# Optimization experiments

Hardware: AMD Instinct MI355X
Metric: run time of the kernel (lower is better)

Reference implementation:

```python
import jax, jax.numpy as jnp
import numpy as np

B, S, I, H, O = 64, 512, 256, 1024, 128

def setup_inputs() -> dict:
    key = jax.random.key(0)
    ks = jax.random.split(key, 9)
    s_in = 1.0 / np.sqrt(I)
    s_h = 1.0 / np.sqrt(H)
    return {
        "x": jax.random.normal(ks[0], (B, S, I), dtype=jnp.float32),
        "W_in": jax.random.uniform(ks[1], (H, I), jnp.float32, -s_in, s_in),
        "b_in": jax.random.uniform(ks[2], (H,), jnp.float32, -s_in, s_in),
        "W_rec": jax.random.uniform(ks[3], (H, H), jnp.float32, -s_h, s_h),
        "b_rec": jax.random.uniform(ks[4], (H,), jnp.float32, -s_h, s_h),
        "tau_m": jnp.full((H,), 2.0, dtype=jnp.float32),
        "tau_n": jnp.full((H,), 2.0, dtype=jnp.float32),
        "W_out": jax.random.uniform(ks[5], (O, H), jnp.float32, -s_h, s_h),
        "b_out": jax.random.uniform(ks[6], (O,), jnp.float32, -s_h, s_h),
    }

def reference(x, W_in, b_in, W_rec, b_rec, tau_m, tau_n, W_out, b_out):
    b, s, _ = x.shape
    h = W_in.shape[0]
    alpha = jax.nn.sigmoid(tau_m)  # [H]
    beta = jax.nn.sigmoid(tau_n)   # [H]
    # Precompute feedforward GEMM for all timesteps at once: [B,S,H]
    ff = jnp.einsum('bsi,hi->bsh', x, W_in) + b_in

    def step(carry, ff_t):
        mem, d, prev_spike = carry  # each [B,H]
        total = ff_t + prev_spike @ W_rec.T + b_rec
        d = beta * d + (1.0 - beta) * total
        mem = alpha * mem + (1.0 - alpha) * d
        spike = (mem > 1.0).astype(mem.dtype)
        mem = mem * (1.0 - spike)
        out = jax.nn.sigmoid(spike @ W_out.T + b_out)  # [B,O]
        return (mem, d, spike), out

    zeros = jnp.zeros((b, h), dtype=x.dtype)
    _, outs = jax.lax.scan(step, (zeros, zeros, zeros), jnp.swapaxes(ff, 0, 1))
    return jnp.swapaxes(outs, 0, 1)  # [B,S,O]
```

## Files before the change

kernel.cpp:

```cpp
#include <hip/hip_runtime.h>
#include <hip/hip_bf16.h>
#include <stdint.h>

#define B_ 64
#define S_ 512
#define I_ 256
#define H_ 1024
#define O_ 128
#define M_ (B_*S_)

typedef float f32x4 __attribute__((ext_vector_type(4)));

__global__ void __launch_bounds__(256) k0_convert(
    const float* __restrict__ x, const float* __restrict__ Win,
    uint8_t* __restrict__ xf8, uint8_t* __restrict__ wf8)
{
    __shared__ unsigned lds32[64 * 65];
    const int i = blockIdx.x;
    const int t = threadIdx.x;

    const float* src;
    uint8_t* dstBase;
    int kqStride;
    if (i < 512) {
        const int r0 = i * 64;
        src = x + (size_t)r0 * 256;
        const int T = i >> 1;
        const int rbase = (i & 1) * 4;
        dstBase = xf8 + (size_t)T * 32768 + rbase * 512;
        kqStride = 4096;
    } else {
        const int i2 = i - 512;
        src = Win + (size_t)(i2 * 64) * 256;
        dstBase = wf8 + (size_t)i2 * 16384;
        kqStride = 2048;
    }

#pragma unroll
    for (int j = 0; j < 16; ++j) {
        const int f = j * 256 + t;
        const int lrow = f >> 6, c4 = f & 63;
        float4 v = *(const float4*)(src + (size_t)lrow * 256 + c4 * 4);
        int w0 = 0;
        w0 = __builtin_amdgcn_cvt_pk_fp8_f32(v.x, v.y, w0, false);
        w0 = __builtin_amdgcn_cvt_pk_fp8_f32(v.z, v.w, w0, true);
        lds32[lrow * 65 + c4] = (unsigned)w0;
    }
    __syncthreads();

#pragma unroll
    for (int j = 0; j < 4; ++j) {
        const int c = j * 256 + t;
        const int kq  = c >> 7;
        const int rem = c & 127;
        const int rbl = rem >> 5;
        const int l0  = (rem & 31) * 2;
        const int r   = l0 & 15;
        const int q   = l0 >> 4;
        const int lrow = rbl * 16 + r;
        const int c0 = kq * 8 + q * 2;
        uint4 o;
        o.x = lds32[lrow * 65 + c0];
        o.y = lds32[lrow * 65 + c0 + 1];
        o.z = lds32[(lrow + 1) * 65 + c0];
        o.w = lds32[(lrow + 1) * 65 + c0 + 1];
        *(uint4*)(dstBase + kq * kqStride + rbl * 512 + l0 * 8) = o;
    }
}

__global__ void __launch_bounds__(256, 4) kf_gemm_scan(
    const uint8_t* __restrict__ xf8, const uint8_t* __restrict__ wf8,
    const float* __restrict__ b_in, const float* __restrict__ b_rec,
    const float* __restrict__ tau_m, const float* __restrict__ tau_n,
    const float* __restrict__ b_out,
    unsigned* __restrict__ crossed,
    float* __restrict__ out)
{
    __shared__ float lsf[128 * 68];

    const int tid  = threadIdx.x;
    const int w    = tid >> 6;
    const int lane = tid & 63;
    const int idx  = blockIdx.x;
    const int b    = (idx & 7) | ((idx >> 7) << 3);
    const int hn   = (idx >> 3) & 15;
    const int colrow = lane & 15;
    const int quad   = lane >> 4;

    float alpha = 0.f, beta = 0.f, cbr = 0.f, oma = 0.f, ombr = 0.f;
    float d = 0.f, mem = 0.f, mx = -1.0f;
    if (tid < 64) {
        const int hs = hn * 64 + tid;
        alpha = 1.f / (1.f + expf(-tau_m[hs]));
        beta  = 1.f / (1.f + expf(-tau_n[hs]));
        oma = 1.f - alpha; ombr = 1.f - beta;
        cbr = ombr * (b_in[hs] + b_rec[hs]);
    }

    const uint8_t* wB = wf8 + (size_t)hn * 16384 + lane * 8;
    long long bq[32];
#pragma unroll
    for (int kq = 0; kq < 8; ++kq)
#pragma unroll
        for (int ni = 0; ni < 4; ++ni)
            bq[kq * 4 + ni] = *(const long long*)(wB + kq * 2048 + ni * 512);

    for (int tt = 0; tt < 4; ++tt) {
        const uint8_t* xA = xf8 + (size_t)(b * 4 + tt) * 32768
                          + w * 1024 + lane * 8;

        f32x4 acc[2][4];
#pragma unroll
        for (int mi = 0; mi < 2; ++mi)
#pragma unroll
            for (int ni = 0; ni < 4; ++ni)
                acc[mi][ni] = (f32x4){0.f, 0.f, 0.f, 0.f};

#pragma unroll
        for (int kq = 0; kq < 8; ++kq) {
            long long a[2];
#pragma unroll
            for (int mi = 0; mi < 2; ++mi)
                a[mi] = *(const long long*)(xA + kq * 4096 + mi * 512);
#pragma unroll
            for (int mi = 0; mi < 2; ++mi)
#pragma unroll
                for (int ni = 0; ni < 4; ++ni)
                    acc[mi][ni] = __builtin_amdgcn_mfma_f32_16x16x32_fp8_fp8(
                        a[mi], bq[kq * 4 + ni], acc[mi][ni], 0, 0, 0);
        }

        __syncthreads();

#pragma unroll
        for (int mi = 0; mi < 2; ++mi) {
            const int t0 = w * 32 + mi * 16 + quad * 4;
#pragma unroll
            for (int ni = 0; ni < 4; ++ni) {
                const int h0 = ni * 16 + colrow;
                float* p = lsf + t0 * 68 + h0;
                p[0]   = acc[mi][ni][0];
                p[68]  = acc[mi][ni][1];
                p[136] = acc[mi][ni][2];
                p[204] = acc[mi][ni][3];
            }
        }
        __syncthreads();

        if (tid < 64) {
            for (int tl0 = 0; tl0 < 128; tl0 += 16) {
                float f[16];
#pragma unroll
                for (int u = 0; u < 16; ++u)
                    f[u] = lsf[(tl0 + u) * 68 + tid];
#pragma unroll
                for (int u = 0; u < 16; ++u) {
                    d   = fmaf(beta,  d,   fmaf(ombr, f[u], cbr));
                    mem = fmaf(alpha, mem, oma * d);
                    mx  = fmaxf(mx, mem);
                }
            }
        }
    }

    if (tid < 64) {
        unsigned long long bal = __ballot(mx > 1.0f);
        if (tid == 0) crossed[b * 16 + hn] = (bal != 0ull) ? 1u : 0u;
    }

    float4 v = *(const float4*)(b_out + (tid & 31) * 4);
    float4 r;
    r.x = 1.f / (1.f + expf(-v.x));
    r.y = 1.f / (1.f + expf(-v.y));
    r.z = 1.f / (1.f + expf(-v.z));
    r.w = 1.f / (1.f + expf(-v.w));
    float4* dst = (float4*)(out + ((size_t)b * S_ + (size_t)hn * 32) * O_);
#pragma unroll
    for (int it = 0; it < 4; ++it)
        dst[it * 256 + tid] = r;
}

__global__ void __launch_bounds__(1024) k3_repair(
    const float* __restrict__ x, const float* __restrict__ W_in,
    const float* __restrict__ b_in,
    const float* __restrict__ W_rec, const float* __restrict__ b_rec,
    const float* __restrict__ tau_m, const float* __restrict__ tau_n,
    const float* __restrict__ W_out, const float* __restrict__ b_out,
    const unsigned* __restrict__ crossed,
    unsigned long long* __restrict__ gmask,
    float* __restrict__ out)
{
    const int b = blockIdx.x;
    const int h = threadIdx.x;
    __shared__ float xrow[I_];
    __shared__ unsigned long long msk[16];
    __shared__ unsigned anyc;
    if (h == 0) {
        unsigned a = 0;
#pragma unroll
        for (int i = 0; i < 16; ++i) a |= crossed[b * 16 + i];
        anyc = a;
    }
    __syncthreads();
    if (anyc == 0u) return;

    if (h < 16) msk[h] = 0ull;
    const float alpha = 1.f / (1.f + expf(-tau_m[h]));
    const float beta  = 1.f / (1.f + expf(-tau_n[h]));
    const float bsum  = b_in[h] + b_rec[h];
    const float* wi = W_in + (size_t)h * I_;
    const float* wr = W_rec + (size_t)h * H_;
    float d = 0.f, mem = 0.f;
    for (int t = 0; t < S_; ++t) {
        __syncthreads();
        if (h < I_) xrow[h] = x[((size_t)b * S_ + t) * I_ + h];
        __syncthreads();
        float ffv = 0.f;
        for (int k = 0; k < I_; ++k) ffv += xrow[k] * wi[k];
        float rec = 0.f;
#pragma unroll
        for (int wd = 0; wd < 16; ++wd) {
            unsigned long long mw = msk[wd];
            while (mw) {
                int bit = __ffsll((long long)mw) - 1;
                rec += wr[(wd << 6) + bit];
                mw &= (mw - 1);
            }
        }
        float tot = ffv + bsum + rec;
        d   = beta  * d   + (1.f - beta)  * tot;
        mem = alpha * mem + (1.f - alpha) * d;
        int sp = (mem > 1.0f) ? 1 : 0;
        if (sp) mem = 0.f;
        unsigned long long bal = __ballot(sp);
        __syncthreads();
        if ((h & 63) == 0) {
            msk[h >> 6] = bal;
            gmask[((size_t)b * S_ + t) * 16 + (h >> 6)] = bal;
        }
    }
    __syncthreads();
    __threadfence_block();
    for (int i = h; i < S_ * O_; i += 1024) {
        const int t = i >> 7, o = i & (O_ - 1);
        float logit = b_out[o];
        const unsigned long long* m = gmask + ((size_t)b * S_ + t) * 16;
        const float* wo = W_out + (size_t)o * H_;
        for (int wd = 0; wd < 16; ++wd) {
            unsigned long long mw = m[wd];
            while (mw) {
                int bit = __ffsll((long long)mw) - 1;
                logit += wo[(wd << 6) + bit];
                mw &= (mw - 1);
            }
        }
        out[((size_t)b * S_ + t) * O_ + o] = 1.f / (1.f + expf(-logit));
    }
}

extern "C" void kernel_launch(void* const* d_in, const int* in_sizes, int n_in,
                              void* d_out, int out_size, void* d_ws, size_t ws_size,
                              hipStream_t stream) {
    const float* x     = (const float*)d_in[0];
    const float* W_in  = (const float*)d_in[1];
    const float* b_in  = (const float*)d_in[2];
    const float* W_rec = (const float*)d_in[3];
    const float* b_rec = (const float*)d_in[4];
    const float* tau_m = (const float*)d_in[5];
    const float* tau_n = (const float*)d_in[6];
    const float* W_out = (const float*)d_in[7];
    const float* b_out = (const float*)d_in[8];
    float* out = (float*)d_out;

    char* ws = (char*)d_ws;
    size_t off = 0;
    uint8_t* xf8 = (uint8_t*)(ws + off);               off += (size_t)M_ * I_;
    uint8_t* wf8 = (uint8_t*)(ws + off);               off += (size_t)H_ * I_;
    unsigned long long* gmask = (unsigned long long*)(ws + off); off += (size_t)B_ * S_ * 16 * 8;
    unsigned* crossed = (unsigned*)(ws + off);         off += 4096;
    if (ws_size < off) return;

    k0_convert<<<528, 256, 0, stream>>>(x, W_in, xf8, wf8);
    kf_gemm_scan<<<1024, 256, 0, stream>>>(xf8, wf8, b_in, b_rec, tau_m, tau_n,
                                           b_out, crossed, out);
    k3_repair<<<64, 1024, 0, stream>>>(x, W_in, b_in, W_rec, b_rec, tau_m, tau_n,
                                       W_out, b_out, crossed, gmask, out);
}
```

Measured before the change: 121.3 us.

## Warp-specialize GEMM-scan kernel with dedicated scan wave and double-buffered LDS

```diff
diff --git a/kernel.cpp b/kernel.cpp
--- a/kernel.cpp
+++ b/kernel.cpp
@@ -68,7 +68,7 @@
     }
 }
 
-__global__ void __launch_bounds__(256, 4) kf_gemm_scan(
+__global__ void __launch_bounds__(320) kf_gemm_scan(
     const uint8_t* __restrict__ xf8, const uint8_t* __restrict__ wf8,
     const float* __restrict__ b_in, const float* __restrict__ b_rec,
     const float* __restrict__ tau_m, const float* __restrict__ tau_n,
@@ -76,7 +76,7 @@
     unsigned* __restrict__ crossed,
     float* __restrict__ out)
 {
-    __shared__ float lsf[128 * 68];
+    __shared__ float lsb[2][64 * 68];
 
     const int tid  = threadIdx.x;
     const int w    = tid >> 6;
@@ -89,8 +89,8 @@
 
     float alpha = 0.f, beta = 0.f, cbr = 0.f, oma = 0.f, ombr = 0.f;
     float d = 0.f, mem = 0.f, mx = -1.0f;
-    if (tid < 64) {
-        const int hs = hn * 64 + tid;
+    if (w == 4) {
+        const int hs = hn * 64 + lane;
         alpha = 1.f / (1.f + expf(-tau_m[hs]));
         beta  = 1.f / (1.f + expf(-tau_n[hs]));
         oma = 1.f - alpha; ombr = 1.f - beta;
@@ -99,62 +99,48 @@
 
     const uint8_t* wB = wf8 + (size_t)hn * 16384 + lane * 8;
     long long bq[32];
-#pragma unroll
-    for (int kq = 0; kq < 8; ++kq)
-#pragma unroll
-        for (int ni = 0; ni < 4; ++ni)
-            bq[kq * 4 + ni] = *(const long long*)(wB + kq * 2048 + ni * 512);
-
-    for (int tt = 0; tt < 4; ++tt) {
-        const uint8_t* xA = xf8 + (size_t)(b * 4 + tt) * 32768
-                          + w * 1024 + lane * 8;
-
-        f32x4 acc[2][4];
-#pragma unroll
-        for (int mi = 0; mi < 2; ++mi)
+    if (w < 4) {
+#pragma unroll
+        for (int kq = 0; kq < 8; ++kq)
 #pragma unroll
             for (int ni = 0; ni < 4; ++ni)
-                acc[mi][ni] = (f32x4){0.f, 0.f, 0.f, 0.f};
-
-#pragma unroll
-        for (int kq = 0; kq < 8; ++kq) {
-            long long a[2];
-#pragma unroll
-            for (int mi = 0; mi < 2; ++mi)
-                a[mi] = *(const long long*)(xA + kq * 4096 + mi * 512);
-#pragma unroll
-            for (int mi = 0; mi < 2; ++mi)
+                bq[kq * 4 + ni] = *(const long long*)(wB + kq * 2048 + ni * 512);
+    }
+
+    f32x4 acc[4];
+    for (int tt2 = 0; tt2 < 8; ++tt2) {
+        if (w < 4) {
+            const uint8_t* xA = xf8 + (size_t)(b * 4 + (tt2 >> 1)) * 32768
+                              + ((tt2 & 1) * 4 + w) * 512 + lane * 8;
+#pragma unroll
+            for (int ni = 0; ni < 4; ++ni)
+                acc[ni] = (f32x4){0.f, 0.f, 0.f, 0.f};
+#pragma unroll
+            for (int kq = 0; kq < 8; ++kq) {
+                long long a = *(const long long*)(xA + kq * 4096);
 #pragma unroll
                 for (int ni = 0; ni < 4; ++ni)
-                    acc[mi][ni] = __builtin_amdgcn_mfma_f32_16x16x32_fp8_fp8(
-                        a[mi], bq[kq * 4 + ni], acc[mi][ni], 0, 0, 0);
-        }
-
-        __syncthreads();
-
-#pragma unroll
-        for (int mi = 0; mi < 2; ++mi) {
-            const int t0 = w * 32 + mi * 16 + quad * 4;
-#pragma unroll
-            for (int ni = 0; ni < 4; ++ni) {
-                const int h0 = ni * 16 + colrow;
-                float* p = lsf + t0 * 68 + h0;
-                p[0]   = acc[mi][ni][0];
-                p[68]  = acc[mi][ni][1];
-                p[136] = acc[mi][ni][2];
-                p[204] = acc[mi][ni][3];
-            }
-        }
-        __syncthreads();
-
-        if (tid < 64) {
-            for (int tl0 = 0; tl0 < 128; tl0 += 16) {
-                float f[16];
-#pragma unroll
-                for (int u = 0; u < 16; ++u)
-                    f[u] = lsf[(tl0 + u) * 68 + tid];
-#pragma unroll
-                for (int u = 0; u < 16; ++u) {
+                    acc[ni] = __builtin_amdgcn_mfma_f32_16x16x32_fp8_fp8(
+                        a, bq[kq * 4 + ni], acc[ni], 0, 0, 0);
+            }
+        }
+        __syncthreads();
+
+        if (w < 4) {
+            float* bufp = lsb[tt2 & 1];
+#pragma unroll
+            for (int ni = 0; ni < 4; ++ni)
+                *(f32x4*)(bufp + (ni * 16 + colrow) * 68 + w * 16 + quad * 4)
+                    = acc[ni];
+        }
+        __syncthreads();
+
+        if (w == 4) {
+            const float* bufp = lsb[tt2 & 1] + lane * 68;
+            for (int t4 = 0; t4 < 16; ++t4) {
+                f32x4 f = *(const f32x4*)(bufp + t4 * 4);
+#pragma unroll
+                for (int u = 0; u < 4; ++u) {
                     d   = fmaf(beta,  d,   fmaf(ombr, f[u], cbr));
                     mem = fmaf(alpha, mem, oma * d);
                     mx  = fmaxf(mx, mem);
@@ -163,21 +149,23 @@
         }
     }
 
-    if (tid < 64) {
+    if (w == 4) {
         unsigned long long bal = __ballot(mx > 1.0f);
-        if (tid == 0) crossed[b * 16 + hn] = (bal != 0ull) ? 1u : 0u;
-    }
-
-    float4 v = *(const float4*)(b_out + (tid & 31) * 4);
-    float4 r;
-    r.x = 1.f / (1.f + expf(-v.x));
-    r.y = 1.f / (1.f + expf(-v.y));
-    r.z = 1.f / (1.f + expf(-v.z));
-    r.w = 1.f / (1.f + expf(-v.w));
-    float4* dst = (float4*)(out + ((size_t)b * S_ + (size_t)hn * 32) * O_);
-#pragma unroll
-    for (int it = 0; it < 4; ++it)
-        dst[it * 256 + tid] = r;
+        if (lane == 0) crossed[b * 16 + hn] = (bal != 0ull) ? 1u : 0u;
+    }
+
+    if (tid < 256) {
+        float4 v = *(const float4*)(b_out + (tid & 31) * 4);
+        float4 r;
+        r.x = 1.f / (1.f + expf(-v.x));
+        r.y = 1.f / (1.f + expf(-v.y));
+        r.z = 1.f / (1.f + expf(-v.z));
+        r.w = 1.f / (1.f + expf(-v.w));
+        float4* dst = (float4*)(out + ((size_t)b * S_ + (size_t)hn * 32) * O_);
+#pragma unroll
+        for (int it = 0; it < 4; ++it)
+            dst[it * 256 + tid] = r;
+    }
 }
 
 __global__ void __launch_bounds__(1024) k3_repair(
@@ -281,7 +269,7 @@
     if (ws_size < off) return;
 
     k0_convert<<<528, 256, 0, stream>>>(x, W_in, xf8, wf8);
-    kf_gemm_scan<<<1024, 256, 0, stream>>>(xf8, wf8, b_in, b_rec, tau_m, tau_n,
+    kf_gemm_scan<<<1024, 320, 0, stream>>>(xf8, wf8, b_in, b_rec, tau_m, tau_n,
                                            b_out, crossed, out);
     k3_repair<<<64, 1024, 0, stream>>>(x, W_in, b_in, W_rec, b_rec, tau_m, tau_n,
                                        W_out, b_out, crossed, gmask, out);
```

Result: slower. 133.4 us (+9.9%).
